# Kernel tuning notes

Measured on AMD Instinct MI355X. Metric: run time of the kernel, lower is better.

Reference implementation:

```python
import jax, jax.numpy as jnp
import numpy as np

NUM_GRAPHS = 512
NODES_PER_GRAPH = 128
HIDDEN = 64
K = 24


def _param(key, shape, scale=0.05):
    return jax.random.normal(key, shape, dtype=jnp.float32) * scale


def setup_inputs() -> dict:
    key = jax.random.key(0)
    ks = jax.random.split(key, 24)
    N = NUM_GRAPHS * NODES_PER_GRAPH
    inp = {
        "x_pf": jax.random.normal(ks[0], (N, 4), dtype=jnp.float32),
        "batch_pf": jnp.repeat(jnp.arange(NUM_GRAPHS, dtype=jnp.int64), NODES_PER_GRAPH),
        # pf_encode: Linear(4,64), ELU, Linear(64,64), ELU
        "we1": _param(ks[1], (4, HIDDEN)), "be1": _param(ks[2], (HIDDEN,)),
        "we2": _param(ks[3], (HIDDEN, HIDDEN)), "be2": _param(ks[4], (HIDDEN,)),
        # three DynamicEdgeConv edge MLPs: Linear(128,64)+ELU
        "wc1": _param(ks[5], (2 * HIDDEN, HIDDEN)), "bc1": _param(ks[6], (HIDDEN,)),
        "wc2": _param(ks[7], (2 * HIDDEN, HIDDEN)), "bc2": _param(ks[8], (HIDDEN,)),
        "wc3": _param(ks[9], (2 * HIDDEN, HIDDEN)), "bc3": _param(ks[10], (HIDDEN,)),
        # output MLP 64->64->32->32->8->1
        "wo1": _param(ks[11], (HIDDEN, 64)), "bo1": _param(ks[12], (64,)),
        "wo2": _param(ks[13], (64, 32)), "bo2": _param(ks[14], (32,)),
        "wo3": _param(ks[15], (32, 32)), "bo3": _param(ks[16], (32,)),
        "wo4": _param(ks[17], (32, 8)), "bo4": _param(ks[18], (8,)),
        "wo5": _param(ks[19], (8, 1)), "bo5": _param(ks[20], (1,)),
    }
    return inp


def dynamic_edge_conv(x, wc, bc):
    """x: [G,P,D]. kNN (incl. self) in feature space per graph, edge feature
    [x_i, x_j - x_i] -> Linear+ELU -> max over neighbors. Matches PyG
    DynamicEdgeConv(nn, k, aggr='max')."""
    sq = jnp.sum(x * x, axis=-1)                                   # [G,P]
    d = sq[:, :, None] + sq[:, None, :] - 2.0 * jnp.einsum('gpd,gqd->gpq', x, x)
    _, idx = jax.lax.top_k(-d, K)                                   # [G,P,K] nearest (self included, dist 0)
    xj = jax.vmap(lambda xg, ig: xg[ig])(x, idx)                    # [G,P,K,D]
    xi = x[:, :, None, :]
    e = jnp.concatenate([jnp.broadcast_to(xi, xj.shape), xj - xi], axis=-1)  # [G,P,K,2D]
    h = jax.nn.elu(e @ wc + bc)                                     # [G,P,K,D]
    return jnp.max(h, axis=2)                                       # [G,P,D]


def reference(x_pf, batch_pf, we1, be1, we2, be2, wc1, bc1, wc2, bc2, wc3, bc3,
              wo1, bo1, wo2, bo2, wo3, bo3, wo4, bo4, wo5, bo5):
    elu = jax.nn.elu
    h = elu(elu(x_pf @ we1 + be1) @ we2 + be2)                      # [N,64]
    h = h.reshape(NUM_GRAPHS, NODES_PER_GRAPH, HIDDEN)              # equal-size graphs
    h = dynamic_edge_conv(h, wc1, bc1)
    h = dynamic_edge_conv(h, wc2, bc2)
    h = dynamic_edge_conv(h, wc3, bc3)
    pooled = jnp.sum(h, axis=1)                                     # global_add_pool -> [G,64]
    o = elu(pooled @ wo1 + bo1)
    o = elu(o @ wo2 + bo2)
    o = elu(o @ wo3 + bo3)
    o = elu(o @ wo4 + bo4)
    out = o @ wo5 + bo5                                             # [G,1]
    return (out, batch_pf)
```

## Files before the change

### kernel.cpp

```cpp
#include <hip/hip_runtime.h>
#include <math.h>

#define NG 512
#define NP 128
#define HID 64
#define KNN 24
#define NTOT (NG*NP)

typedef __attribute__((ext_vector_type(8)))  short  short8;
typedef __attribute__((ext_vector_type(16))) float  floatx16;

__device__ __forceinline__ float elu_f(float v) { return v > 0.0f ? v : expm1f(v); }

__device__ __forceinline__ void split_bf16(float x, unsigned short& hb, unsigned short& lb) {
    unsigned u = __float_as_uint(x);
    unsigned h = (u + 0x7FFFu + ((u >> 16) & 1u)) >> 16;
    hb = (unsigned short)h;
    float hf = __uint_as_float(h << 16);
    float lo = x - hf;
    unsigned v = __float_as_uint(lo);
    lb = (unsigned short)((v + 0x7FFFu + ((v >> 16) & 1u)) >> 16);
}
__device__ __forceinline__ unsigned short bf_rne(float x) {
    unsigned u = __float_as_uint(x);
    return (unsigned short)((u + 0x7FFFu + ((u >> 16) & 1u)) >> 16);
}
__device__ __forceinline__ float bf_lo(unsigned u) { return __uint_as_float(u << 16); }
__device__ __forceinline__ float bf_hi(unsigned u) { return __uint_as_float(u & 0xFFFF0000u); }

__device__ __forceinline__ unsigned short f_to_key(unsigned short b) {
    return (unsigned short)(b ^ ((b & 0x8000u) ? 0xFFFFu : 0x8000u));
}
__device__ __forceinline__ float key_to_f(unsigned k) {
    const unsigned bf = (k & 0x8000u) ? (k ^ 0x8000u) : (k ^ 0xFFFFu);
    return __uint_as_float(bf << 16);
}
__device__ __forceinline__ unsigned pk_max_u16(unsigned a, unsigned b) {
    unsigned d;
    asm("v_pk_max_u16 %0, %1, %2" : "=v"(d) : "v"(a), "v"(b));
    return d;
}

__device__ __forceinline__ unsigned short* hchunk(unsigned short* base, int row, int ch) {
    return base + (((row << 4) + (ch ^ (row & 15))) << 3);
}
__device__ __forceinline__ const unsigned short* hchunk(const unsigned short* base, int row, int ch) {
    return base + (((row << 4) + (ch ^ (row & 15))) << 3);
}

__device__ __forceinline__ void sort8_asc(unsigned* y) {
    #pragma unroll
    for (int k = 2; k <= 8; k <<= 1)
        #pragma unroll
        for (int j = k >> 1; j > 0; j >>= 1)
            #pragma unroll
            for (int i = 0; i < 8; ++i) {
                const int l = i ^ j;
                if (l > i) {
                    const bool up = ((i & k) == 0);
                    const unsigned a = y[i], b = y[l];
                    const unsigned mn = a < b ? a : b;
                    const unsigned mx = a < b ? b : a;
                    y[i] = up ? mn : mx;
                    y[l] = up ? mx : mn;
                }
            }
}

__device__ __forceinline__ void merge_top24(unsigned* x) {
    #pragma unroll
    for (int d = 16; d > 0; d >>= 1)
        #pragma unroll
        for (int i = 0; i < 32; ++i)
            if (!(i & d) && i < 24) {
                const int l = i | d;
                const unsigned a = x[i], b = x[l];
                x[i] = a < b ? a : b;
                x[l] = a < b ? b : a;
            }
}

__global__ __launch_bounds__(256) void pack_w(
    const float* __restrict__ wc1, const float* __restrict__ wc2, const float* __restrict__ wc3,
    const float* __restrict__ we2,
    unsigned short* __restrict__ wp)
{
    const int n = blockIdx.x*256 + threadIdx.x;
    if (n < 24576) {
        const int layer = n >> 13;
        const int r = n & 8191;
        const int e = r & 7, j = (r >> 3) & 127, ch = r >> 10;
        const int k = (ch >> 1)*16 + (ch & 1)*8 + e;
        const float* wc = (layer == 0) ? wc1 : ((layer == 1) ? wc2 : wc3);
        float w;
        if (j < 64) w = wc[k*64 + j] - wc[(k+64)*64 + j];
        else        w = wc[(k+64)*64 + (j-64)];
        unsigned short hb, lb;
        split_bf16(w, hb, lb);
        unsigned short* base = wp + layer*16384;
        base[r] = hb;
        base[8192 + r] = lb;
    } else if (n < 24576 + 4096) {
        const int m = n - 24576;
        const int e = m & 7, col = (m >> 3) & 63, ch = m >> 9;
        const int k = (ch >> 1)*16 + (ch & 1)*8 + e;
        unsigned short hb, lb;
        split_bf16(we2[k*64 + col], hb, lb);
        unsigned short* base = wp + 49152;
        base[m] = hb;
        base[4096 + m] = lb;
    }
}

__global__ __launch_bounds__(512, 4) void conv_all(
    const float* __restrict__ x,
    const unsigned short* __restrict__ wp,
    const float* __restrict__ bc1, const float* __restrict__ bc2, const float* __restrict__ bc3,
    const float* __restrict__ we1, const float* __restrict__ be1,
    const unsigned short* __restrict__ we2p, const float* __restrict__ be2,
    float* __restrict__ ag_all, float* __restrict__ pooled_out, float* __restrict__ out_batch)
{
    __shared__ __align__(16) char arena[53760];
    unsigned*        keys  = (unsigned*)arena;
    unsigned*        nnidx = (unsigned*)(arena + 17408);
    unsigned short*  hilo  = (unsigned short*)(arena + 20480);
    float*           sqs   = (float*)(arena + 53248);

    const int g = blockIdx.x;
    const int t = threadIdx.x;
    const int w = t >> 6, lane = t & 63;
    const int lj = lane & 31, half = lane >> 5;
    const int rt = w & 3, wg = w >> 2;
    const int i2 = t & 127, s4 = t >> 7;
    float* __restrict__ ag = ag_all + (size_t)g * (NP*HID);

    {
        float* w1s = (float*)arena;
        float* b1v = (float*)(arena + 1024);
        float* b2v = (float*)(arena + 1280);
        if (t < 256) w1s[t] = we1[t];
        else if (t < 320) b1v[t-256] = be1[t-256];
        else if (t < 384) b2v[t-320] = be2[t-320];
        if (t < 128) out_batch[(size_t)g*128 + t] = (float)g;
        __syncthreads();

        const int n = t & 127, fh = t >> 7, f0 = fh*16;
        const float4 xv = ((const float4*)x)[g*128 + n];
        float acc1[16];
        #pragma unroll
        for (int q = 0; q < 4; ++q) {
            const float4 b4 = *(const float4*)(b1v + f0 + q*4);
            acc1[q*4+0] = b4.x; acc1[q*4+1] = b4.y; acc1[q*4+2] = b4.z; acc1[q*4+3] = b4.w;
        }
        #pragma unroll
        for (int k = 0; k < 4; ++k) {
            const float xk_ = (k == 0) ? xv.x : (k == 1) ? xv.y : (k == 2) ? xv.z : xv.w;
            #pragma unroll
            for (int q = 0; q < 4; ++q) {
                const float4 w4 = *(const float4*)(w1s + k*64 + f0 + q*4);
                acc1[q*4+0] = fmaf(xk_, w4.x, acc1[q*4+0]);
                acc1[q*4+1] = fmaf(xk_, w4.y, acc1[q*4+1]);
                acc1[q*4+2] = fmaf(xk_, w4.z, acc1[q*4+2]);
                acc1[q*4+3] = fmaf(xk_, w4.w, acc1[q*4+3]);
            }
        }
        unsigned hu[8], lu[8];
        #pragma unroll
        for (int e = 0; e < 8; ++e) {
            const float v0 = elu_f(acc1[2*e]), v1 = elu_f(acc1[2*e+1]);
            unsigned short h0, l0, h1, l1;
            split_bf16(v0, h0, l0); split_bf16(v1, h1, l1);
            hu[e] = (unsigned)h0 | ((unsigned)h1 << 16);
            lu[e] = (unsigned)l0 | ((unsigned)l1 << 16);
        }
        *(uint4*)hchunk(hilo, n, fh*2)       = make_uint4(hu[0], hu[1], hu[2], hu[3]);
        *(uint4*)hchunk(hilo, n, fh*2 + 1)   = make_uint4(hu[4], hu[5], hu[6], hu[7]);
        *(uint4*)hchunk(hilo, n, 8 + fh*2)   = make_uint4(lu[0], lu[1], lu[2], lu[3]);
        *(uint4*)hchunk(hilo, n, 8 + fh*2+1) = make_uint4(lu[4], lu[5], lu[6], lu[7]);
        __syncthreads();

        const int jt2 = wg;
        floatx16 acc = {0.f,0.f,0.f,0.f,0.f,0.f,0.f,0.f,0.f,0.f,0.f,0.f,0.f,0.f,0.f,0.f};
        #pragma unroll
        for (int p = 0; p < 3; ++p) {
            const int aSel = (p == 2) ? 8 : 0;
            const int part = (p == 1) ? 1 : 0;
            short8 af[4], bf4[4];
            #pragma unroll
            for (int c = 0; c < 4; ++c) {
                af[c]  = *(const short8*)hchunk(hilo, rt*32 + lj, aSel + c*2 + half);
                bf4[c] = *(const short8*)((const short*)we2p + part*4096 + (((c*2 + half)*64) + jt2*32 + lj)*8);
            }
            #pragma unroll
            for (int c = 0; c < 4; ++c) acc = __builtin_amdgcn_mfma_f32_32x32x16_bf16(af[c], bf4[c], acc, 0, 0, 0);
        }
        const int col = jt2*32 + lj;
        const float bias = b2v[col];
        __syncthreads();
        #pragma unroll
        for (int reg = 0; reg < 16; ++reg) {
            const int row = (reg & 3) + 8*(reg >> 2) + 4*half + rt*32;
            const float v = elu_f(acc[reg] + bias);
            unsigned short hb, lb;
            split_bf16(v, hb, lb);
            *(hchunk(hilo, row, col >> 3) + (col & 7))       = hb;
            *(hchunk(hilo, row, 8 + (col >> 3)) + (col & 7)) = lb;
        }
        __syncthreads();

        const int r = t >> 2, cq = t & 3, c0 = cq*2;
        const uint4 h0 = *(const uint4*)hchunk(hilo, r, c0);
        const uint4 h1 = *(const uint4*)hchunk(hilo, r, c0+1);
        const uint4 l0 = *(const uint4*)hchunk(hilo, r, 8+c0);
        const uint4 l1 = *(const uint4*)hchunk(hilo, r, 8+c0+1);
        float s = 0.0f;
        const unsigned hh[8] = {h0.x,h0.y,h0.z,h0.w,h1.x,h1.y,h1.z,h1.w};
        const unsigned ll[8] = {l0.x,l0.y,l0.z,l0.w,l1.x,l1.y,l1.z,l1.w};
        #pragma unroll
        for (int e = 0; e < 8; ++e) {
            const float va = bf_lo(hh[e]) + bf_lo(ll[e]);
            const float vb = bf_hi(hh[e]) + bf_hi(ll[e]);
            s = fmaf(va, va, s); s = fmaf(vb, vb, s);
        }
        s += __shfl_xor(s, 1);
        s += __shfl_xor(s, 2);
        if (cq == 0) sqs[r] = s;
        __syncthreads();
    }

    #pragma unroll 1
    for (int L = 0; L < 3; ++L) {
        const unsigned short* wpl = wp + L*16384;
        const float* bcl = (L == 0) ? bc1 : (L == 1) ? bc2 : bc3;

        unsigned xk[32];
        #pragma unroll
        for (int s = 0; s < 24; ++s) xk[s] = 0xFFFFFFFFu;

        #pragma unroll 1
        for (int jt = 0; jt < 4; ++jt) {
            if (wg == (jt & 1)) {
                floatx16 acc = {0.f,0.f,0.f,0.f,0.f,0.f,0.f,0.f,0.f,0.f,0.f,0.f,0.f,0.f,0.f,0.f};
                #pragma unroll
                for (int p = 0; p < 3; ++p) {
                    const int aSel = (p == 2) ? 8 : 0;
                    const int bSel = (p == 1) ? 8 : 0;
                    short8 af[4], bf4[4];
                    #pragma unroll
                    for (int c = 0; c < 4; ++c) {
                        af[c]  = *(const short8*)hchunk(hilo, rt*32 + lj, aSel + c*2 + half);
                        bf4[c] = *(const short8*)hchunk(hilo, jt*32 + lj, bSel + c*2 + half);
                    }
                    #pragma unroll
                    for (int c = 0; c < 4; ++c) acc = __builtin_amdgcn_mfma_f32_32x32x16_bf16(af[c], bf4[c], acc, 0, 0, 0);
                }
                const unsigned jg = (unsigned)(jt*32 + lj);
                const float sqj = sqs[jg];
                #pragma unroll
                for (int reg = 0; reg < 16; ++reg) {
                    const int i = (reg & 3) + 8*(reg >> 2) + 4*half + rt*32;
                    float d = fmaf(-2.0f, acc[reg], sqs[i] + sqj);
                    d = fmaxf(d, 0.0f);
                    keys[i*33 + lj] = (__float_as_uint(d) & 0xFFFFFF80u) | jg;
                }
            }
            __syncthreads();
            {
                const unsigned* kr = keys + i2*33 + s4*8;
                const uint4 k0 = *(const uint4*)kr;
                const uint4 k1 = *(const uint4*)(kr + 4);
                unsigned y[8] = {k0.x, k0.y, k0.z, k0.w, k1.x, k1.y, k1.z, k1.w};
                sort8_asc(y);
                #pragma unroll
                for (int e = 0; e < 8; ++e) xk[24+e] = y[7-e];
                merge_top24(xk);
            }
            __syncthreads();
        }

        #pragma unroll 1
        for (int src = 1; src < 4; ++src) {
            if (s4 == src) {
                #pragma unroll
                for (int e = 0; e < 24; ++e) keys[i2*33 + 9 + e] = xk[e];
            }
            __syncthreads();
            if (s4 == 0) {
                #pragma unroll 1
                for (int b = 0; b < 3; ++b) {
                    #pragma unroll
                    for (int e = 0; e < 8; ++e) xk[24+e] = keys[i2*33 + 9 + b*8 + (7-e)];
                    merge_top24(xk);
                }
            }
            __syncthreads();
        }
        if (s4 == 0) {
            #pragma unroll
            for (int c = 0; c < 6; ++c)
                nnidx[i2*6 + c] = (xk[c*4] & 127u) | ((xk[c*4+1] & 127u) << 8)
                                | ((xk[c*4+2] & 127u) << 16) | ((xk[c*4+3] & 127u) << 24);
        }
        __syncthreads();

        unsigned short* bs = (unsigned short*)arena;
        {
            short8 afr[8];
            #pragma unroll
            for (int sel = 0; sel < 2; ++sel)
                #pragma unroll
                for (int c = 0; c < 4; ++c)
                    afr[sel*4+c] = *(const short8*)hchunk(hilo, rt*32 + lj, sel*8 + c*2 + half);

            #pragma unroll 1
            for (int q2 = 0; q2 < 2; ++q2) {
                const int jt = wg*2 + q2;
                short8 bfr[8];
                #pragma unroll
                for (int part = 0; part < 2; ++part)
                    #pragma unroll
                    for (int c = 0; c < 4; ++c)
                        bfr[part*4+c] = *(const short8*)((const short*)wpl + part*8192 + (((c*2 + half)*128) + jt*32 + lj)*8);
                floatx16 acc = {0.f,0.f,0.f,0.f,0.f,0.f,0.f,0.f,0.f,0.f,0.f,0.f,0.f,0.f,0.f,0.f};
                #pragma unroll
                for (int c = 0; c < 4; ++c) acc = __builtin_amdgcn_mfma_f32_32x32x16_bf16(afr[c],   bfr[c],   acc, 0, 0, 0);
                #pragma unroll
                for (int c = 0; c < 4; ++c) acc = __builtin_amdgcn_mfma_f32_32x32x16_bf16(afr[c],   bfr[4+c], acc, 0, 0, 0);
                #pragma unroll
                for (int c = 0; c < 4; ++c) acc = __builtin_amdgcn_mfma_f32_32x32x16_bf16(afr[4+c], bfr[c],   acc, 0, 0, 0);

                if (wg == 0) {
                    const int col = jt*32 + lj;
                    const float bias = bcl[col];
                    #pragma unroll
                    for (int reg = 0; reg < 16; ++reg) {
                        const int row = (reg & 3) + 8*(reg >> 2) + 4*half + rt*32;
                        ag[(size_t)row*64 + col] = acc[reg] + bias;
                    }
                } else {
                    const int colb = q2*32 + lj;
                    #pragma unroll
                    for (int reg = 0; reg < 16; ++reg) {
                        const int row = (reg & 3) + 8*(reg >> 2) + 4*half + rt*32;
                        bs[row*68 + colb] = f_to_key(bf_rne(acc[reg]));
                    }
                }
            }
        }
        __syncthreads();

        {
            const int q = lane >> 4, fq = lane & 15;
            float4 psum = make_float4(0.f, 0.f, 0.f, 0.f);
            #pragma unroll 1
            for (int rg = 0; rg < 4; ++rg) {
                const int row = w*16 + rg*4 + q;
                unsigned mk0 = 0u, mk1 = 0u;
                #pragma unroll
                for (int c = 0; c < 6; ++c) {
                    const unsigned pk = nnidx[row*6 + c];
                    #pragma unroll
                    for (int e = 0; e < 4; ++e) {
                        const int j = (pk >> (8*e)) & 127;
                        const uint2 bb = *(const uint2*)(bs + j*68 + fq*4);
                        mk0 = pk_max_u16(mk0, bb.x);
                        mk1 = pk_max_u16(mk1, bb.y);
                    }
                }
                const float4 av = *(const float4*)(ag + (size_t)row*64 + fq*4);
                float4 o;
                o.x = elu_f(av.x + key_to_f(mk0 & 0xFFFFu));
                o.y = elu_f(av.y + key_to_f(mk0 >> 16));
                o.z = elu_f(av.z + key_to_f(mk1 & 0xFFFFu));
                o.w = elu_f(av.w + key_to_f(mk1 >> 16));

                if (L < 2) {
                    unsigned short hx,lx,hy,ly,hz,lz,hw2,lw2;
                    split_bf16(o.x,hx,lx); split_bf16(o.y,hy,ly);
                    split_bf16(o.z,hz,lz); split_bf16(o.w,hw2,lw2);
                    *(uint2*)(hchunk(hilo, row, fq >> 1) + (fq & 1)*4) =
                        make_uint2((unsigned)hx | ((unsigned)hy << 16), (unsigned)hz | ((unsigned)hw2 << 16));
                    *(uint2*)(hchunk(hilo, row, 8 + (fq >> 1)) + (fq & 1)*4) =
                        make_uint2((unsigned)lx | ((unsigned)ly << 16), (unsigned)lz | ((unsigned)lw2 << 16));
                    float sp = o.x*o.x + o.y*o.y + o.z*o.z + o.w*o.w;
                    sp += __shfl_xor(sp, 1);
                    sp += __shfl_xor(sp, 2);
                    sp += __shfl_xor(sp, 4);
                    sp += __shfl_xor(sp, 8);
                    if (fq == 0) sqs[row] = sp;
                } else {
                    psum.x += o.x; psum.y += o.y; psum.z += o.z; psum.w += o.w;
                }
            }
            if (L < 2) {
                __syncthreads();
            } else {
                __syncthreads();
                float* pool8 = (float*)(arena + 17408);
                psum.x += __shfl_xor(psum.x, 16); psum.y += __shfl_xor(psum.y, 16);
                psum.z += __shfl_xor(psum.z, 16); psum.w += __shfl_xor(psum.w, 16);
                psum.x += __shfl_xor(psum.x, 32); psum.y += __shfl_xor(psum.y, 32);
                psum.z += __shfl_xor(psum.z, 32); psum.w += __shfl_xor(psum.w, 32);
                if (q == 0) *(float4*)(pool8 + w*64 + fq*4) = psum;
                __syncthreads();
                if (t < 64) {
                    float s = 0.0f;
                    #pragma unroll
                    for (int k = 0; k < 8; ++k) s += pool8[k*64 + t];
                    pooled_out[(size_t)g*64 + t] = s;
                }
            }
        }
    }
}

__global__ __launch_bounds__(64) void head_kernel(
    const float* __restrict__ pooled_in,
    const float* __restrict__ wo1, const float* __restrict__ bo1,
    const float* __restrict__ wo2, const float* __restrict__ bo2,
    const float* __restrict__ wo3, const float* __restrict__ bo3,
    const float* __restrict__ wo4, const float* __restrict__ bo4,
    const float* __restrict__ wo5, const float* __restrict__ bo5,
    float* __restrict__ outp)
{
    __shared__ float pooled[64];
    __shared__ float o1[64];
    __shared__ float o2[32];
    __shared__ float o3[32];
    __shared__ float o4[8];
    const int g = blockIdx.x, t = threadIdx.x;

    pooled[t] = pooled_in[(size_t)g*64 + t];
    {
        float acc = bo1[t];
        #pragma unroll
        for (int k = 0; k < 64; ++k) acc = fmaf(pooled[k], wo1[k*64 + t], acc);
        o1[t] = elu_f(acc);
    }
    if (t < 32) {
        float acc = bo2[t];
        #pragma unroll
        for (int k = 0; k < 64; ++k) acc = fmaf(o1[k], wo2[k*32 + t], acc);
        o2[t] = elu_f(acc);
    }
    if (t < 32) {
        float acc = bo3[t];
        #pragma unroll
        for (int k = 0; k < 32; ++k) acc = fmaf(o2[k], wo3[k*32 + t], acc);
        o3[t] = elu_f(acc);
    }
    if (t < 8) {
        float acc = bo4[t];
        #pragma unroll
        for (int k = 0; k < 32; ++k) acc = fmaf(o3[k], wo4[k*8 + t], acc);
        o4[t] = elu_f(acc);
    }
    if (t == 0) {
        float acc = bo5[0];
        #pragma unroll
        for (int k = 0; k < 8; ++k) acc = fmaf(o4[k], wo5[k], acc);
        outp[g] = acc;
    }
}

extern "C" void kernel_launch(void* const* d_in, const int* in_sizes, int n_in,
                              void* d_out, int out_size, void* d_ws, size_t ws_size,
                              hipStream_t stream) {
    const float* x_pf = (const float*)d_in[0];
    const float* we1 = (const float*)d_in[2];
    const float* be1 = (const float*)d_in[3];
    const float* we2 = (const float*)d_in[4];
    const float* be2 = (const float*)d_in[5];
    const float* wc1 = (const float*)d_in[6];
    const float* bc1 = (const float*)d_in[7];
    const float* wc2 = (const float*)d_in[8];
    const float* bc2 = (const float*)d_in[9];
    const float* wc3 = (const float*)d_in[10];
    const float* bc3 = (const float*)d_in[11];
    const float* wo1 = (const float*)d_in[12];
    const float* bo1 = (const float*)d_in[13];
    const float* wo2 = (const float*)d_in[14];
    const float* bo2 = (const float*)d_in[15];
    const float* wo3 = (const float*)d_in[16];
    const float* bo3 = (const float*)d_in[17];
    const float* wo4 = (const float*)d_in[18];
    const float* bo4 = (const float*)d_in[19];
    const float* wo5 = (const float*)d_in[20];
    const float* bo5 = (const float*)d_in[21];

    float* out = (float*)d_out;
    char* ws = (char*)d_ws;
    float* abuf   = (float*)(ws);
    float* pooled = (float*)(ws + (size_t)16*1024*1024);
    unsigned short* wpack = (unsigned short*)(ws + (size_t)17*1024*1024);

    pack_w<<<112, 256, 0, stream>>>(wc1, wc2, wc3, we2, wpack);

    conv_all<<<NG, 512, 0, stream>>>(x_pf, wpack, bc1, bc2, bc3,
        we1, be1, wpack + 49152, be2, abuf, pooled, out + NG);

    head_kernel<<<NG, 64, 0, stream>>>(pooled, wo1, bo1, wo2, bo2, wo3, bo3, wo4, bo4, wo5, bo5, out);
}
```

Baseline: 186.9 us.

## Restructure kNN top-k selection into two wide passes with shuffle-based merging

The distance tiling is rearranged so both warp groups compute 64 columns at once into a wider key buffer, cutting the column passes from four to two. Each row is now handled by four adjacent lanes that each keep a partial top-24. Those partials are combined with two xor-shuffle bitonic merges instead of the earlier serial shared-memory rounds, where one quarter of the threads merged while the rest waited. This removes several barriers and idle-thread phases. In exchange, LDS per block grows from about 53 KB to 69 KB, which may reduce how many blocks fit per CU, and register pressure rises.

New measurement: 181.4 us. -3.0%, faster.

```diff
diff --git a/kernel.cpp b/kernel.cpp
--- a/kernel.cpp
+++ b/kernel.cpp
@@ -78,6 +78,27 @@
                 x[i] = a < b ? a : b;
                 x[l] = a < b ? b : a;
             }
+}
+
+__device__ __forceinline__ void merge2_shfl(unsigned* xk, int mask) {
+    unsigned z[32];
+    #pragma unroll
+    for (int e = 0; e < 24; ++e) {
+        const unsigned ye = (unsigned)__shfl_xor((int)xk[23 - e], mask);
+        z[8 + e] = xk[e] < ye ? xk[e] : ye;
+    }
+    #pragma unroll
+    for (int d = 16; d > 0; d >>= 1)
+        #pragma unroll
+        for (int i = 8; i < 32; ++i)
+            if (!(i & d)) {
+                const int l = i | d;
+                const unsigned a = z[i], b = z[l];
+                z[i] = a < b ? a : b;
+                z[l] = a < b ? b : a;
+            }
+    #pragma unroll
+    for (int e = 0; e < 24; ++e) xk[e] = z[8 + e];
 }
 
 __global__ __launch_bounds__(256) void pack_w(
@@ -120,18 +141,17 @@
     const unsigned short* __restrict__ we2p, const float* __restrict__ be2,
     float* __restrict__ ag_all, float* __restrict__ pooled_out, float* __restrict__ out_batch)
 {
-    __shared__ __align__(16) char arena[53760];
+    __shared__ __align__(16) char arena[69632];
     unsigned*        keys  = (unsigned*)arena;
-    unsigned*        nnidx = (unsigned*)(arena + 17408);
-    unsigned short*  hilo  = (unsigned short*)(arena + 20480);
-    float*           sqs   = (float*)(arena + 53248);
+    unsigned*        nnidx = (unsigned*)(arena + 33280);
+    unsigned short*  hilo  = (unsigned short*)(arena + 36352);
+    float*           sqs   = (float*)(arena + 69120);
 
     const int g = blockIdx.x;
     const int t = threadIdx.x;
     const int w = t >> 6, lane = t & 63;
     const int lj = lane & 31, half = lane >> 5;
     const int rt = w & 3, wg = w >> 2;
-    const int i2 = t & 127, s4 = t >> 7;
     float* __restrict__ ag = ag_all + (size_t)g * (NP*HID);
 
     {
@@ -173,6 +193,7 @@
             hu[e] = (unsigned)h0 | ((unsigned)h1 << 16);
             lu[e] = (unsigned)l0 | ((unsigned)l1 << 16);
         }
+        __syncthreads();
         *(uint4*)hchunk(hilo, n, fh*2)       = make_uint4(hu[0], hu[1], hu[2], hu[3]);
         *(uint4*)hchunk(hilo, n, fh*2 + 1)   = make_uint4(hu[4], hu[5], hu[6], hu[7]);
         *(uint4*)hchunk(hilo, n, 8 + fh*2)   = make_uint4(lu[0], lu[1], lu[2], lu[3]);
@@ -195,7 +216,7 @@
             for (int c = 0; c < 4; ++c) acc = __builtin_amdgcn_mfma_f32_32x32x16_bf16(af[c], bf4[c], acc, 0, 0, 0);
         }
         const int col = jt2*32 + lj;
-        const float bias = b2v[col];
+        const float bias = ((const float*)(arena + 1280))[col];
         __syncthreads();
         #pragma unroll
         for (int reg = 0; reg < 16; ++reg) {
@@ -238,8 +259,9 @@
         for (int s = 0; s < 24; ++s) xk[s] = 0xFFFFFFFFu;
 
         #pragma unroll 1
-        for (int jt = 0; jt < 4; ++jt) {
-            if (wg == (jt & 1)) {
+        for (int r = 0; r < 2; ++r) {
+            const int jt = r*2 + wg;
+            {
                 floatx16 acc = {0.f,0.f,0.f,0.f,0.f,0.f,0.f,0.f,0.f,0.f,0.f,0.f,0.f,0.f,0.f,0.f};
                 #pragma unroll
                 for (int p = 0; p < 3; ++p) {
@@ -261,47 +283,42 @@
                     const int i = (reg & 3) + 8*(reg >> 2) + 4*half + rt*32;
                     float d = fmaf(-2.0f, acc[reg], sqs[i] + sqj);
                     d = fmaxf(d, 0.0f);
-                    keys[i*33 + lj] = (__float_as_uint(d) & 0xFFFFFF80u) | jg;
+                    keys[i*65 + wg*32 + lj] = (__float_as_uint(d) & 0xFFFFFF80u) | jg;
                 }
             }
             __syncthreads();
             {
-                const unsigned* kr = keys + i2*33 + s4*8;
+                const unsigned* kr = keys + (t >> 2)*65 + (t & 3)*16;
                 const uint4 k0 = *(const uint4*)kr;
                 const uint4 k1 = *(const uint4*)(kr + 4);
-                unsigned y[8] = {k0.x, k0.y, k0.z, k0.w, k1.x, k1.y, k1.z, k1.w};
-                sort8_asc(y);
-                #pragma unroll
-                for (int e = 0; e < 8; ++e) xk[24+e] = y[7-e];
-                merge_top24(xk);
+                {
+                    unsigned y[8] = {k0.x, k0.y, k0.z, k0.w, k1.x, k1.y, k1.z, k1.w};
+                    sort8_asc(y);
+                    #pragma unroll
+                    for (int e = 0; e < 8; ++e) xk[24+e] = y[7-e];
+                    merge_top24(xk);
+                }
+                const uint4 k2 = *(const uint4*)(kr + 8);
+                const uint4 k3 = *(const uint4*)(kr + 12);
+                {
+                    unsigned y[8] = {k2.x, k2.y, k2.z, k2.w, k3.x, k3.y, k3.z, k3.w};
+                    sort8_asc(y);
+                    #pragma unroll
+                    for (int e = 0; e < 8; ++e) xk[24+e] = y[7-e];
+                    merge_top24(xk);
+                }
             }
             __syncthreads();
         }
 
-        #pragma unroll 1
-        for (int src = 1; src < 4; ++src) {
-            if (s4 == src) {
-                #pragma unroll
-                for (int e = 0; e < 24; ++e) keys[i2*33 + 9 + e] = xk[e];
-            }
-            __syncthreads();
-            if (s4 == 0) {
-                #pragma unroll 1
-                for (int b = 0; b < 3; ++b) {
-                    #pragma unroll
-                    for (int e = 0; e < 8; ++e) xk[24+e] = keys[i2*33 + 9 + b*8 + (7-e)];
-                    merge_top24(xk);
-                }
-            }
-            __syncthreads();
-        }
-        if (s4 == 0) {
+        merge2_shfl(xk, 1);
+        merge2_shfl(xk, 2);
+        if ((t & 3) == 0) {
             #pragma unroll
             for (int c = 0; c < 6; ++c)
-                nnidx[i2*6 + c] = (xk[c*4] & 127u) | ((xk[c*4+1] & 127u) << 8)
-                                | ((xk[c*4+2] & 127u) << 16) | ((xk[c*4+3] & 127u) << 24);
-        }
-        __syncthreads();
+                nnidx[(t >> 2)*6 + c] = (xk[c*4] & 127u) | ((xk[c*4+1] & 127u) << 8)
+                                      | ((xk[c*4+2] & 127u) << 16) | ((xk[c*4+3] & 127u) << 24);
+        }
 
         unsigned short* bs = (unsigned short*)arena;
         {
@@ -396,7 +413,7 @@
                 __syncthreads();
             } else {
                 __syncthreads();
-                float* pool8 = (float*)(arena + 17408);
+                float* pool8 = (float*)(arena + 33280);
                 psum.x += __shfl_xor(psum.x, 16); psum.y += __shfl_xor(psum.y, 16);
                 psum.z += __shfl_xor(psum.z, 16); psum.w += __shfl_xor(psum.w, 16);
                 psum.x += __shfl_xor(psum.x, 32); psum.y += __shfl_xor(psum.y, 32);
```
